# Kernel tuning notes

Measured on AMD Instinct MI355X. Metric: run time of the kernel, lower is better.

The kernel has to match this reference:

```python
import jax, jax.numpy as jnp
import numpy as np

EPS = 1e-6

def setup_inputs() -> dict:
    key = jax.random.key(0)
    k1, k2, k3 = jax.random.split(key, 3)
    B, C, H, W = 2048, 256, 7, 7
    base = jax.random.normal(k1, (B, C, H, W), dtype=jnp.float32)
    moment = jax.random.normal(k2, (B, C, H, W), dtype=jnp.float32)
    A_matrix = jax.random.randint(k3, (B, H * W, H * W), 0, 2, dtype=jnp.int32)
    return {"base": base, "moment": moment, "A_matrix": A_matrix}

def reference(base, moment, A_matrix):
    B, C, H, W = base.shape
    P = H * W  # 49
    b = base.reshape(B, C, P)      # (B, C, 49)
    m = moment.reshape(B, C, P)    # (B, C, 49)
    # pairwise dot over channel dim via batched matmul (avoids BxCx49x49 broadcast)
    dots = jnp.einsum('bcp,bcq->bpq', b, m)            # (B, 49, 49)
    nb = jnp.maximum(jnp.linalg.norm(b, axis=1), EPS)  # (B, 49)
    nm = jnp.maximum(jnp.linalg.norm(m, axis=1), EPS)  # (B, 49)
    cos_sim = dots / (nb[:, :, None] * nm[:, None, :])
    mask = A_matrix.astype(bool)
    # masked mean without dynamic-size gather
    num = jnp.sum(jnp.where(mask, cos_sim, 0.0))
    den = jnp.sum(mask).astype(cos_sim.dtype)
    return -(num / den)
```

## Files before the change

### kernel.cpp

```cpp
#include <hip/hip_runtime.h>
#include <stdint.h>


typedef __attribute__((ext_vector_type(8))) short short8;
typedef __attribute__((ext_vector_type(4))) float floatx4;

#define P 49
#define C 256
#define CP 12544
#define NMASK 2401
#define LDST 264

__device__ __forceinline__ uint16_t f2bf_rne(float f) {
  union { float f; uint32_t u; } x; x.f = f;
  uint32_t u = x.u;
  u += 0x7FFFu + ((u >> 16) & 1u);
  return (uint16_t)(u >> 16);
}
__device__ __forceinline__ float bf2f(uint16_t h) {
  union { uint32_t u; float f; } x; x.u = ((uint32_t)h) << 16;
  return x.f;
}

__global__ __launch_bounds__(256) void pixpro_main(
    const float* __restrict__ base, const float* __restrict__ moment,
    const int* __restrict__ A, float* __restrict__ ws_num, float* __restrict__ ws_cnt)
{
  __shared__ uint16_t lb[P * LDST];
  __shared__ uint16_t lm[P * LDST];
  __shared__ float inv_nb[P], inv_nm[P];
  __shared__ float red[8];

  const int b    = blockIdx.x;
  const int tid  = threadIdx.x;
  const int lane = tid & 63;
  const int wv   = tid >> 6;

  const float* gb = base   + (size_t)b * CP;
  const float* gm = moment + (size_t)b * CP;

  for (int arr = 0; arr < 2; ++arr) {
    const float* g = arr ? gm : gb;
    uint16_t*    l = arr ? lm : lb;
    for (int t = tid; t < 32 * P; t += 256) {
      int p  = t % P;
      int c0 = (t / P) * 8;
      float v[8];
      #pragma unroll
      for (int j = 0; j < 8; ++j) v[j] = g[(c0 + j) * P + p];
      union { uint16_t u[8]; short8 s; } pk;
      #pragma unroll
      for (int j = 0; j < 8; ++j) pk.u[j] = f2bf_rne(v[j]);
      *(short8*)&l[p * LDST + c0] = pk.s;
    }
  }
  __syncthreads();

  if (wv < 2 && lane < P) {
    const uint16_t* row = (wv ? lm : lb) + lane * LDST;
    float s = 0.f;
    #pragma unroll 4
    for (int c8 = 0; c8 < 32; ++c8) {
      union { short8 s; uint16_t u[8]; } v;
      v.s = *(const short8*)&row[c8 * 8];
      #pragma unroll
      for (int j = 0; j < 8; ++j) { float f = bf2f(v.u[j]); s += f * f; }
    }
    float inv = 1.0f / fmaxf(sqrtf(s), 1e-6f);
    (wv ? inv_nm : inv_nb)[lane] = inv;
  }
  __syncthreads();

  const int tbase[4] = {0, 16, 32, 33};
  const int pb   = tbase[wv];
  const int mrow = lane & 15;
  const int kgrp = lane >> 4;

  short8 afrag[8];
  #pragma unroll
  for (int kk = 0; kk < 8; ++kk)
    afrag[kk] = *(const short8*)&lb[(pb + mrow) * LDST + kk * 32 + kgrp * 8];

  float local_num = 0.f;
  int   local_cnt = 0;

  #pragma unroll
  for (int qt = 0; qt < 4; ++qt) {
    const int qb = tbase[qt];
    floatx4 acc = {0.f, 0.f, 0.f, 0.f};
    #pragma unroll
    for (int kk = 0; kk < 8; ++kk) {
      short8 bfrag = *(const short8*)&lm[(qb + mrow) * LDST + kk * 32 + kgrp * 8];
      acc = __builtin_amdgcn_mfma_f32_16x16x32_bf16(afrag[kk], bfrag, acc, 0, 0, 0);
    }
    const int  q      = qb + mrow;
    const bool qvalid = (qt < 3) || (q == 48);
    const float inm   = inv_nm[q];
    #pragma unroll
    for (int r = 0; r < 4; ++r) {
      const int  p      = pb + kgrp * 4 + r;
      const bool pvalid = (wv < 3) || (p == 48);
      if (pvalid && qvalid) {
        int mval = A[(size_t)b * NMASK + p * P + q];
        if (mval != 0) {
          local_num += acc[r] * inv_nb[p] * inm;
          local_cnt += 1;
        }
      }
    }
  }

  #pragma unroll
  for (int off = 32; off > 0; off >>= 1) {
    local_num += __shfl_down(local_num, off, 64);
    local_cnt += __shfl_down(local_cnt, off, 64);
  }
  if (lane == 0) { red[wv] = local_num; red[4 + wv] = (float)local_cnt; }
  __syncthreads();
  if (tid == 0) {
    ws_num[b] = red[0] + red[1] + red[2] + red[3];
    ws_cnt[b] = red[4] + red[5] + red[6] + red[7];
  }
}

__global__ __launch_bounds__(256) void pixpro_reduce(
    const float* __restrict__ ws_num, const float* __restrict__ ws_cnt,
    float* __restrict__ out)
{
  __shared__ float rn[4], rc[4];
  float n = 0.f, c = 0.f;
  for (int i = threadIdx.x; i < 2048; i += 256) { n += ws_num[i]; c += ws_cnt[i]; }
  #pragma unroll
  for (int off = 32; off > 0; off >>= 1) {
    n += __shfl_down(n, off, 64);
    c += __shfl_down(c, off, 64);
  }
  const int wv = threadIdx.x >> 6, lane = threadIdx.x & 63;
  if (lane == 0) { rn[wv] = n; rc[wv] = c; }
  __syncthreads();
  if (threadIdx.x == 0) {
    float N = rn[0] + rn[1] + rn[2] + rn[3];
    float D = rc[0] + rc[1] + rc[2] + rc[3];
    out[0] = -(N / D);
  }
}

extern "C" void kernel_launch(void* const* d_in, const int* in_sizes, int n_in,
                              void* d_out, int out_size, void* d_ws, size_t ws_size,
                              hipStream_t stream) {
  const float* base   = (const float*)d_in[0];
  const float* moment = (const float*)d_in[1];
  const int*   A      = (const int*)d_in[2];
  float* ws_num = (float*)d_ws;
  float* ws_cnt = ws_num + 2048;
  pixpro_main<<<2048, 256, 0, stream>>>(base, moment, A, ws_num, ws_cnt);
  pixpro_reduce<<<1, 256, 0, stream>>>(ws_num, ws_cnt, (float*)d_out);
}
```

Before: 252.5 us.

## Double block size, batch global loads and mask prefetch, fuse norms into MFMA loop

Each block now uses 512 threads (8 waves), with each wave computing two of the four q tiles for its p tile. All global loads of base, moment and the mask are issued up front into registers before conversion to bf16, so more memory requests are in flight. The separate norm pass and its extra barrier are removed: row norms are computed from the MFMA fragments already loaded and reduced with lane shuffles. In exchange, register pressure goes up and the moment norms are recomputed redundantly by waves that share a q tile.

```diff
diff --git a/kernel.cpp b/kernel.cpp
--- a/kernel.cpp
+++ b/kernel.cpp
@@ -6,7 +6,6 @@
 typedef __attribute__((ext_vector_type(4))) float floatx4;
 
 #define P 49
-#define C 256
 #define CP 12544
 #define NMASK 2401
 #define LDST 264
@@ -22,14 +21,13 @@
   return x.f;
 }
 
-__global__ __launch_bounds__(256) void pixpro_main(
+__global__ __launch_bounds__(512, 6) void pixpro_main(
     const float* __restrict__ base, const float* __restrict__ moment,
     const int* __restrict__ A, float* __restrict__ ws_num, float* __restrict__ ws_cnt)
 {
   __shared__ uint16_t lb[P * LDST];
   __shared__ uint16_t lm[P * LDST];
-  __shared__ float inv_nb[P], inv_nm[P];
-  __shared__ float red[8];
+  __shared__ float red[16];
 
   const int b    = blockIdx.x;
   const int tid  = threadIdx.x;
@@ -39,73 +37,107 @@
   const float* gb = base   + (size_t)b * CP;
   const float* gm = moment + (size_t)b * CP;
 
-  for (int arr = 0; arr < 2; ++arr) {
-    const float* g = arr ? gm : gb;
-    uint16_t*    l = arr ? lm : lb;
-    for (int t = tid; t < 32 * P; t += 256) {
-      int p  = t % P;
-      int c0 = (t / P) * 8;
-      float v[8];
-      #pragma unroll
-      for (int j = 0; j < 8; ++j) v[j] = g[(c0 + j) * P + p];
-      union { uint16_t u[8]; short8 s; } pk;
-      #pragma unroll
-      for (int j = 0; j < 8; ++j) pk.u[j] = f2bf_rne(v[j]);
-      *(short8*)&l[p * LDST + c0] = pk.s;
+  float vb[3][8], vm[3][8];
+  int pp[3], cc[3];
+  #pragma unroll
+  for (int k = 0; k < 3; ++k) {
+    int t = tid + 512 * k;
+    pp[k] = t % P;
+    cc[k] = (t / P) * 8;
+    const float* g0 = gb + cc[k] * P + pp[k];
+    #pragma unroll
+    for (int j = 0; j < 8; ++j) vb[k][j] = g0[j * P];
+  }
+  #pragma unroll
+  for (int k = 0; k < 3; ++k) {
+    const float* g1 = gm + cc[k] * P + pp[k];
+    #pragma unroll
+    for (int j = 0; j < 8; ++j) vm[k][j] = g1[j * P];
+  }
+
+  const int mrow = lane & 15;
+  const int kgrp = lane >> 4;
+  const int pt   = wv & 3;
+  const int qt0  = (wv >> 2) * 2;
+  const int pb   = (pt == 3) ? 33 : 16 * pt;
+  int mv[2][4];
+  #pragma unroll
+  for (int s = 0; s < 2; ++s) {
+    int qt = qt0 + s;
+    int qb = (qt == 3) ? 33 : 16 * qt;
+    int q  = qb + mrow;
+    const int* Ab = A + (size_t)b * NMASK + q;
+    #pragma unroll
+    for (int r = 0; r < 4; ++r) {
+      int p = pb + kgrp * 4 + r;
+      mv[s][r] = Ab[p * P];
     }
+  }
+
+  #pragma unroll
+  for (int k = 0; k < 3; ++k) {
+    union { uint16_t u[8]; short8 s8; } pk;
+    #pragma unroll
+    for (int j = 0; j < 8; ++j) pk.u[j] = f2bf_rne(vb[k][j]);
+    *(short8*)&lb[pp[k] * LDST + cc[k]] = pk.s8;
+    #pragma unroll
+    for (int j = 0; j < 8; ++j) pk.u[j] = f2bf_rne(vm[k][j]);
+    *(short8*)&lm[pp[k] * LDST + cc[k]] = pk.s8;
+  }
+  if (tid < 32) {
+    int t = 1536 + tid;
+    int p = t % P, c0 = (t / P) * 8;
+    union { uint16_t u[8]; short8 s8; } pk;
+    #pragma unroll
+    for (int j = 0; j < 8; ++j) pk.u[j] = f2bf_rne(gb[(c0 + j) * P + p]);
+    *(short8*)&lb[p * LDST + c0] = pk.s8;
+    #pragma unroll
+    for (int j = 0; j < 8; ++j) pk.u[j] = f2bf_rne(gm[(c0 + j) * P + p]);
+    *(short8*)&lm[p * LDST + c0] = pk.s8;
   }
   __syncthreads();
 
-  if (wv < 2 && lane < P) {
-    const uint16_t* row = (wv ? lm : lb) + lane * LDST;
-    float s = 0.f;
-    #pragma unroll 4
-    for (int c8 = 0; c8 < 32; ++c8) {
-      union { short8 s; uint16_t u[8]; } v;
-      v.s = *(const short8*)&row[c8 * 8];
-      #pragma unroll
-      for (int j = 0; j < 8; ++j) { float f = bf2f(v.u[j]); s += f * f; }
-    }
-    float inv = 1.0f / fmaxf(sqrtf(s), 1e-6f);
-    (wv ? inv_nm : inv_nb)[lane] = inv;
+  short8 afrag[8];
+  float sb = 0.f;
+  #pragma unroll
+  for (int kk = 0; kk < 8; ++kk) {
+    afrag[kk] = *(const short8*)&lb[(pb + mrow) * LDST + kk * 32 + kgrp * 8];
+    #pragma unroll
+    for (int j = 0; j < 8; ++j) { float f = bf2f((uint16_t)afrag[kk][j]); sb = fmaf(f, f, sb); }
   }
-  __syncthreads();
-
-  const int tbase[4] = {0, 16, 32, 33};
-  const int pb   = tbase[wv];
-  const int mrow = lane & 15;
-  const int kgrp = lane >> 4;
-
-  short8 afrag[8];
+  sb += __shfl_xor(sb, 16, 64);
+  sb += __shfl_xor(sb, 32, 64);
+  const float inv_nb_own = 1.0f / fmaxf(sqrtf(sb), 1e-6f);
+  float inv_nb_r[4];
   #pragma unroll
-  for (int kk = 0; kk < 8; ++kk)
-    afrag[kk] = *(const short8*)&lb[(pb + mrow) * LDST + kk * 32 + kgrp * 8];
+  for (int r = 0; r < 4; ++r) inv_nb_r[r] = __shfl(inv_nb_own, kgrp * 4 + r, 64);
 
   float local_num = 0.f;
   int   local_cnt = 0;
 
   #pragma unroll
-  for (int qt = 0; qt < 4; ++qt) {
-    const int qb = tbase[qt];
+  for (int s = 0; s < 2; ++s) {
+    const int qt = qt0 + s;
+    const int qb = (qt == 3) ? 33 : 16 * qt;
     floatx4 acc = {0.f, 0.f, 0.f, 0.f};
+    float sm = 0.f;
     #pragma unroll
     for (int kk = 0; kk < 8; ++kk) {
       short8 bfrag = *(const short8*)&lm[(qb + mrow) * LDST + kk * 32 + kgrp * 8];
+      #pragma unroll
+      for (int j = 0; j < 8; ++j) { float f = bf2f((uint16_t)bfrag[j]); sm = fmaf(f, f, sm); }
       acc = __builtin_amdgcn_mfma_f32_16x16x32_bf16(afrag[kk], bfrag, acc, 0, 0, 0);
     }
-    const int  q      = qb + mrow;
-    const bool qvalid = (qt < 3) || (q == 48);
-    const float inm   = inv_nm[q];
+    sm += __shfl_xor(sm, 16, 64);
+    sm += __shfl_xor(sm, 32, 64);
+    const float inv_nm_own = 1.0f / fmaxf(sqrtf(sm), 1e-6f);
+    const bool qvalid = (qt < 3) || (mrow == 15);
     #pragma unroll
     for (int r = 0; r < 4; ++r) {
-      const int  p      = pb + kgrp * 4 + r;
-      const bool pvalid = (wv < 3) || (p == 48);
-      if (pvalid && qvalid) {
-        int mval = A[(size_t)b * NMASK + p * P + q];
-        if (mval != 0) {
-          local_num += acc[r] * inv_nb[p] * inm;
-          local_cnt += 1;
-        }
+      const bool pvalid = (pt < 3) || (kgrp * 4 + r == 15);
+      if (pvalid && qvalid && mv[s][r] != 0) {
+        local_num += acc[r] * inv_nb_r[r] * inv_nm_own;
+        local_cnt += 1;
       }
     }
   }
@@ -115,11 +147,13 @@
     local_num += __shfl_down(local_num, off, 64);
     local_cnt += __shfl_down(local_cnt, off, 64);
   }
-  if (lane == 0) { red[wv] = local_num; red[4 + wv] = (float)local_cnt; }
+  if (lane == 0) { red[wv] = local_num; red[8 + wv] = (float)local_cnt; }
   __syncthreads();
   if (tid == 0) {
-    ws_num[b] = red[0] + red[1] + red[2] + red[3];
-    ws_cnt[b] = red[4] + red[5] + red[6] + red[7];
+    float n = 0.f, c = 0.f;
+    #pragma unroll
+    for (int i = 0; i < 8; ++i) { n += red[i]; c += red[8 + i]; }
+    ws_num[b] = n; ws_cnt[b] = c;
   }
 }
 
@@ -153,6 +187,6 @@
   const int*   A      = (const int*)d_in[2];
   float* ws_num = (float*)d_ws;
   float* ws_cnt = ws_num + 2048;
-  pixpro_main<<<2048, 256, 0, stream>>>(base, moment, A, ws_num, ws_cnt);
+  pixpro_main<<<2048, 512, 0, stream>>>(base, moment, A, ws_num, ws_cnt);
   pixpro_reduce<<<1, 256, 0, stream>>>(ws_num, ws_cnt, (float*)d_out);
 }
```

After: 235.4 us. -6.8%, faster.

## Reassociate masked cosine sum as moment·(mask·inv_norm) matmul then dot with base

Applied to the files above, without the earlier changes.

Reorders the computation: it first forms a masked, norm-scaled mask matrix (mask[p,q]*inv_nm[q]) in bf16 and multiplies moment (C×49) by it with MFMA. The result is then dotted with base in fp32 directly from global memory, and base norms are computed along the way. This removes the transposed strided global load and bf16 staging of both tensors into LDS, and moves to 512 threads per block with vectorized row loads. The trade-off is that the mask times inverse norm is now rounded to bf16, which changes numerical error, and the base reads are scattered scalar global loads.

```diff
diff --git a/kernel.cpp b/kernel.cpp
--- a/kernel.cpp
+++ b/kernel.cpp
@@ -1,4 +1,5 @@
 #include <hip/hip_runtime.h>
+#include <hip/hip_bf16.h>
 #include <stdint.h>
 
 
@@ -6,120 +7,214 @@
 typedef __attribute__((ext_vector_type(4))) float floatx4;
 
 #define P 49
-#define C 256
 #define CP 12544
 #define NMASK 2401
-#define LDST 264
-
-__device__ __forceinline__ uint16_t f2bf_rne(float f) {
-  union { float f; uint32_t u; } x; x.f = f;
-  uint32_t u = x.u;
-  u += 0x7FFFu + ((u >> 16) & 1u);
-  return (uint16_t)(u >> 16);
-}
-__device__ __forceinline__ float bf2f(uint16_t h) {
-  union { uint32_t u; float f; } x; x.u = ((uint32_t)h) << 16;
-  return x.f;
-}
-
-__global__ __launch_bounds__(256) void pixpro_main(
+#define MS_STRIDE 72
+
+__device__ __forceinline__ short8 cvt8(float4 a, float4 b) {
+  union { __hip_bfloat162 h2; short s2[2]; } t;
+  short8 r;
+  t.h2 = __float22bfloat162_rn(make_float2(a.x, a.y)); r[0] = t.s2[0]; r[1] = t.s2[1];
+  t.h2 = __float22bfloat162_rn(make_float2(a.z, a.w)); r[2] = t.s2[0]; r[3] = t.s2[1];
+  t.h2 = __float22bfloat162_rn(make_float2(b.x, b.y)); r[4] = t.s2[0]; r[5] = t.s2[1];
+  t.h2 = __float22bfloat162_rn(make_float2(b.z, b.w)); r[6] = t.s2[0]; r[7] = t.s2[1];
+  return r;
+}
+
+__global__ __launch_bounds__(512, 6) void pixpro_main(
     const float* __restrict__ base, const float* __restrict__ moment,
     const int* __restrict__ A, float* __restrict__ ws_num, float* __restrict__ ws_cnt)
 {
-  __shared__ uint16_t lb[P * LDST];
-  __shared__ uint16_t lm[P * LDST];
-  __shared__ float inv_nb[P], inv_nm[P];
-  __shared__ float red[8];
+  __shared__ __align__(16) uint16_t maskS[P * MS_STRIDE];
+  __shared__ __align__(16) float normred[8 * 4 * 64];
+  __shared__ __align__(16) float inv_nm_s[64];
+  __shared__ __align__(16) float SQred[8 * 4 * 16 * 2];
+  __shared__ float cntred[8];
 
   const int b    = blockIdx.x;
   const int tid  = threadIdx.x;
   const int lane = tid & 63;
   const int wv   = tid >> 6;
+  const int mrow = lane & 15;
+  const int kgrp = (lane >> 4) & 3;
 
   const float* gb = base   + (size_t)b * CP;
   const float* gm = moment + (size_t)b * CP;
-
-  for (int arr = 0; arr < 2; ++arr) {
-    const float* g = arr ? gm : gb;
-    uint16_t*    l = arr ? lm : lb;
-    for (int t = tid; t < 32 * P; t += 256) {
-      int p  = t % P;
-      int c0 = (t / P) * 8;
-      float v[8];
-      #pragma unroll
-      for (int j = 0; j < 8; ++j) v[j] = g[(c0 + j) * P + p];
-      union { uint16_t u[8]; short8 s; } pk;
-      #pragma unroll
-      for (int j = 0; j < 8; ++j) pk.u[j] = f2bf_rne(v[j]);
-      *(short8*)&l[p * LDST + c0] = pk.s;
-    }
-  }
-  __syncthreads();
-
-  if (wv < 2 && lane < P) {
-    const uint16_t* row = (wv ? lm : lb) + lane * LDST;
+  const int*   gA = A      + (size_t)b * NMASK;
+
+  short8 afrag[2][2];
+  float s0[8], s1[8];
+  #pragma unroll
+  for (int j = 0; j < 8; ++j) { s0[j] = 0.f; s1[j] = 0.f; }
+
+  #pragma unroll
+  for (int cti = 0; cti < 2; ++cti) {
+    const int c = (2 * wv + cti) * 16 + mrow;
+    const float* row = gm + c * P;
+    float4 a0 = *(const float4*)(row + kgrp * 8);
+    float4 a1 = *(const float4*)(row + kgrp * 8 + 4);
+    float4 b0, b1;
+    if (kgrp < 2) {
+      b0 = *(const float4*)(row + 32 + kgrp * 8);
+      b1 = *(const float4*)(row + 32 + kgrp * 8 + 4);
+    } else if (kgrp == 2) {
+      b0 = make_float4(row[48], 0.f, 0.f, 0.f);
+      b1 = make_float4(0.f, 0.f, 0.f, 0.f);
+    } else {
+      b0 = make_float4(0.f, 0.f, 0.f, 0.f);
+      b1 = make_float4(0.f, 0.f, 0.f, 0.f);
+    }
+    s0[0] = fmaf(a0.x, a0.x, s0[0]); s0[1] = fmaf(a0.y, a0.y, s0[1]);
+    s0[2] = fmaf(a0.z, a0.z, s0[2]); s0[3] = fmaf(a0.w, a0.w, s0[3]);
+    s0[4] = fmaf(a1.x, a1.x, s0[4]); s0[5] = fmaf(a1.y, a1.y, s0[5]);
+    s0[6] = fmaf(a1.z, a1.z, s0[6]); s0[7] = fmaf(a1.w, a1.w, s0[7]);
+    s1[0] = fmaf(b0.x, b0.x, s1[0]); s1[1] = fmaf(b0.y, b0.y, s1[1]);
+    s1[2] = fmaf(b0.z, b0.z, s1[2]); s1[3] = fmaf(b0.w, b0.w, s1[3]);
+    s1[4] = fmaf(b1.x, b1.x, s1[4]); s1[5] = fmaf(b1.y, b1.y, s1[5]);
+    s1[6] = fmaf(b1.z, b1.z, s1[6]); s1[7] = fmaf(b1.w, b1.w, s1[7]);
+    afrag[cti][0] = cvt8(a0, a1);
+    afrag[cti][1] = cvt8(b0, b1);
+  }
+
+  const bool btask = tid < P * 8;
+  const int  bp    = tid >> 3;
+  const int  bqg   = tid & 7;
+  const int  bq0   = bqg * 8;
+  int bmask[8];
+  #pragma unroll
+  for (int j = 0; j < 8; ++j) bmask[j] = 0;
+  if (btask) {
+    const int* Ar = gA + bp * P + bq0;
+    if (bqg <= 5) {
+      int4 u0 = *(const int4*)(Ar);
+      int4 u1 = *(const int4*)(Ar + 4);
+      bmask[0] = u0.x; bmask[1] = u0.y; bmask[2] = u0.z; bmask[3] = u0.w;
+      bmask[4] = u1.x; bmask[5] = u1.y; bmask[6] = u1.z; bmask[7] = u1.w;
+    } else if (bqg == 6) {
+      bmask[0] = Ar[0];
+    }
+  }
+
+  #pragma unroll
+  for (int j = 0; j < 8; ++j) {
+    s0[j] += __shfl_xor(s0[j], 1); s0[j] += __shfl_xor(s0[j], 2);
+    s1[j] += __shfl_xor(s1[j], 1); s1[j] += __shfl_xor(s1[j], 2);
+  }
+  if ((lane & 3) == 0) {
+    const int h = mrow >> 2;
+    float* nb_ = &normred[(wv * 4 + h) * 64 + kgrp * 8];
+    *(float4*)(nb_ + 0)  = make_float4(s0[0], s0[1], s0[2], s0[3]);
+    *(float4*)(nb_ + 4)  = make_float4(s0[4], s0[5], s0[6], s0[7]);
+    *(float4*)(nb_ + 32) = make_float4(s1[0], s1[1], s1[2], s1[3]);
+    *(float4*)(nb_ + 36) = make_float4(s1[4], s1[5], s1[6], s1[7]);
+  }
+  __syncthreads();
+
+  if (tid < 64) {
     float s = 0.f;
-    #pragma unroll 4
-    for (int c8 = 0; c8 < 32; ++c8) {
-      union { short8 s; uint16_t u[8]; } v;
-      v.s = *(const short8*)&row[c8 * 8];
-      #pragma unroll
-      for (int j = 0; j < 8; ++j) { float f = bf2f(v.u[j]); s += f * f; }
-    }
-    float inv = 1.0f / fmaxf(sqrtf(s), 1e-6f);
-    (wv ? inv_nm : inv_nb)[lane] = inv;
-  }
-  __syncthreads();
-
-  const int tbase[4] = {0, 16, 32, 33};
-  const int pb   = tbase[wv];
-  const int mrow = lane & 15;
-  const int kgrp = lane >> 4;
-
-  short8 afrag[8];
-  #pragma unroll
-  for (int kk = 0; kk < 8; ++kk)
-    afrag[kk] = *(const short8*)&lb[(pb + mrow) * LDST + kk * 32 + kgrp * 8];
-
-  float local_num = 0.f;
-  int   local_cnt = 0;
-
-  #pragma unroll
-  for (int qt = 0; qt < 4; ++qt) {
-    const int qb = tbase[qt];
-    floatx4 acc = {0.f, 0.f, 0.f, 0.f};
-    #pragma unroll
-    for (int kk = 0; kk < 8; ++kk) {
-      short8 bfrag = *(const short8*)&lm[(qb + mrow) * LDST + kk * 32 + kgrp * 8];
-      acc = __builtin_amdgcn_mfma_f32_16x16x32_bf16(afrag[kk], bfrag, acc, 0, 0, 0);
-    }
-    const int  q      = qb + mrow;
-    const bool qvalid = (qt < 3) || (q == 48);
-    const float inm   = inv_nm[q];
-    #pragma unroll
-    for (int r = 0; r < 4; ++r) {
-      const int  p      = pb + kgrp * 4 + r;
-      const bool pvalid = (wv < 3) || (p == 48);
-      if (pvalid && qvalid) {
-        int mval = A[(size_t)b * NMASK + p * P + q];
-        if (mval != 0) {
-          local_num += acc[r] * inv_nb[p] * inm;
-          local_cnt += 1;
-        }
+    #pragma unroll
+    for (int wh = 0; wh < 32; ++wh) s += normred[wh * 64 + tid];
+    inv_nm_s[tid] = 1.0f / fmaxf(sqrtf(s), 1e-6f);
+  }
+  __syncthreads();
+
+  int cntpart = 0;
+  if (btask) {
+    float4 i0 = *(const float4*)&inv_nm_s[bq0];
+    float4 i1 = *(const float4*)&inv_nm_s[bq0 + 4];
+    float4 f0, f1;
+    f0.x = bmask[0] ? i0.x : 0.f; f0.y = bmask[1] ? i0.y : 0.f;
+    f0.z = bmask[2] ? i0.z : 0.f; f0.w = bmask[3] ? i0.w : 0.f;
+    f1.x = bmask[4] ? i1.x : 0.f; f1.y = bmask[5] ? i1.y : 0.f;
+    f1.z = bmask[6] ? i1.z : 0.f; f1.w = bmask[7] ? i1.w : 0.f;
+    #pragma unroll
+    for (int j = 0; j < 8; ++j) cntpart += bmask[j];
+    *(short8*)&maskS[bp * MS_STRIDE + bq0] = cvt8(f0, f1);
+  }
+  __syncthreads();
+
+  const int pbase[4] = {0, 16, 32, 33};
+  floatx4 acc[2][4];
+  #pragma unroll
+  for (int i = 0; i < 2; ++i)
+    #pragma unroll
+    for (int j = 0; j < 4; ++j) acc[i][j] = (floatx4){0.f, 0.f, 0.f, 0.f};
+
+  #pragma unroll
+  for (int kt = 0; kt < 2; ++kt) {
+    short8 bfr[4];
+    #pragma unroll
+    for (int pt = 0; pt < 4; ++pt)
+      bfr[pt] = *(const short8*)&maskS[(pbase[pt] + mrow) * MS_STRIDE + kt * 32 + kgrp * 8];
+    #pragma unroll
+    for (int cti = 0; cti < 2; ++cti)
+      #pragma unroll
+      for (int pt = 0; pt < 4; ++pt)
+        acc[cti][pt] = __builtin_amdgcn_mfma_f32_16x16x32_bf16(afrag[cti][kt], bfr[pt], acc[cti][pt], 0, 0, 0);
+  }
+
+  float S[4] = {0.f, 0.f, 0.f, 0.f}, Qn[4] = {0.f, 0.f, 0.f, 0.f};
+  #pragma unroll
+  for (int cti = 0; cti < 2; ++cti) {
+    float bv[4][4];
+    #pragma unroll
+    for (int pt = 0; pt < 4; ++pt) {
+      const int pd = pbase[pt] + mrow;
+      const bool pv = (pt < 3) || (mrow == 15);
+      #pragma unroll
+      for (int r = 0; r < 4; ++r) {
+        const int c = (2 * wv + cti) * 16 + kgrp * 4 + r;
+        float v = gb[c * P + pd];
+        bv[pt][r] = pv ? v : 0.f;
       }
     }
-  }
-
-  #pragma unroll
-  for (int off = 32; off > 0; off >>= 1) {
-    local_num += __shfl_down(local_num, off, 64);
-    local_cnt += __shfl_down(local_cnt, off, 64);
-  }
-  if (lane == 0) { red[wv] = local_num; red[4 + wv] = (float)local_cnt; }
-  __syncthreads();
-  if (tid == 0) {
-    ws_num[b] = red[0] + red[1] + red[2] + red[3];
-    ws_cnt[b] = red[4] + red[5] + red[6] + red[7];
+    #pragma unroll
+    for (int pt = 0; pt < 4; ++pt)
+      #pragma unroll
+      for (int r = 0; r < 4; ++r) {
+        S[pt]  = fmaf(bv[pt][r], acc[cti][pt][r], S[pt]);
+        Qn[pt] = fmaf(bv[pt][r], bv[pt][r], Qn[pt]);
+      }
+  }
+
+  #pragma unroll
+  for (int pt = 0; pt < 4; ++pt) {
+    S[pt]  += __shfl_xor(S[pt], 16);  S[pt]  += __shfl_xor(S[pt], 32);
+    Qn[pt] += __shfl_xor(Qn[pt], 16); Qn[pt] += __shfl_xor(Qn[pt], 32);
+  }
+  float cntf = (float)cntpart;
+  #pragma unroll
+  for (int off = 32; off > 0; off >>= 1) cntf += __shfl_xor(cntf, off);
+
+  if (lane < 16) {
+    #pragma unroll
+    for (int pt = 0; pt < 4; ++pt)
+      *(float2*)&SQred[((wv * 4 + pt) * 16 + mrow) * 2] = make_float2(S[pt], Qn[pt]);
+  }
+  if (lane == 0) cntred[wv] = cntf;
+  __syncthreads();
+
+  if (tid < 64) {
+    float num = 0.f, cc = 0.f;
+    if (tid < P) {
+      const int pt = tid >> 4;
+      const int mr = (pt == 3) ? 15 : (tid & 15);
+      float Sp = 0.f, Qp = 0.f;
+      #pragma unroll
+      for (int w = 0; w < 8; ++w) {
+        const int idx = ((w * 4 + pt) * 16 + mr) * 2;
+        Sp += SQred[idx];
+        Qp += SQred[idx + 1];
+      }
+      num = Sp * (1.0f / fmaxf(sqrtf(Qp), 1e-6f));
+    }
+    if (tid < 8) cc = cntred[tid];
+    #pragma unroll
+    for (int off = 32; off > 0; off >>= 1) {
+      num += __shfl_xor(num, off);
+      cc  += __shfl_xor(cc, off);
+    }
+    if (tid == 0) { ws_num[b] = num; ws_cnt[b] = cc; }
   }
 }
 
@@ -153,6 +248,6 @@
   const int*   A      = (const int*)d_in[2];
   float* ws_num = (float*)d_ws;
   float* ws_cnt = ws_num + 2048;
-  pixpro_main<<<2048, 256, 0, stream>>>(base, moment, A, ws_num, ws_cnt);
+  pixpro_main<<<2048, 512, 0, stream>>>(base, moment, A, ws_num, ws_cnt);
   pixpro_reduce<<<1, 256, 0, stream>>>(ws_num, ws_cnt, (float*)d_out);
 }
```

Result: faster. 235.3 us (-6.8%).
